# Optimization experiments

Measured on AMD Instinct MI355X. Metric: run time of the kernel, lower is better.

Reference implementation:

```python
import jax, jax.numpy as jnp
import numpy as np

NUM_HEADS = 12
GAT_HEADS = 4
EPS = 1e-5

def _ln(x, g, b):
    m = x.mean(-1, keepdims=True)
    v = ((x - m) ** 2).mean(-1, keepdims=True)
    return (x - m) / jnp.sqrt(v + EPS) * g + b

def _grid_edges(H, W, B):
    # 8-ish connectivity exactly as the Python loops build it: horizontal,
    # vertical, down-right diag, down-left diag (c>0), both directions,
    # replicated per image with node offset. Pure numpy on static shapes.
    idx = np.arange(H * W).reshape(H, W)
    p = [np.stack([idx[:, :-1].ravel(), idx[:, 1:].ravel()], 1),
         np.stack([idx[:-1, :].ravel(), idx[1:, :].ravel()], 1),
         np.stack([idx[:-1, :-1].ravel(), idx[1:, 1:].ravel()], 1),
         np.stack([idx[:-1, 1:-1].ravel(), idx[1:, :-2].ravel()], 1)]
    e = np.concatenate(p, 0)
    e = np.concatenate([e, e[:, ::-1]], 0)  # bidirectional
    e = (e[None] + (np.arange(B) * H * W)[:, None, None]).reshape(-1, 2)
    return jnp.asarray(e[:, 0]), jnp.asarray(e[:, 1])

def _forward(x, ln1_g, ln1_b, proj_w, proj_b, wqkv, bqkv, wo, bo, ln2_g, ln2_b,
             gp_w, gp_b, gat_w, att_src, att_dst, gat_b, ln3_g, ln3_b,
             mlp_w1, mlp_b1, mlp_w2, mlp_b2, fn_g, fn_b):
    B, C, H, W = x.shape
    S = H * W
    E = proj_w.shape[1]
    tok = x.reshape(B, C, S).transpose(0, 2, 1)            # [B,S,C]
    v_in = _ln(tok, ln1_g, ln1_b) @ proj_w + proj_b        # [B,S,E]
    # --- multi-head self-attention (batch_first, eval: no dropout) ---
    qkv = v_in @ wqkv + bqkv
    q, k, v = jnp.split(qkv, 3, axis=-1)
    dh = E // NUM_HEADS
    def heads(t):
        return t.reshape(B, S, NUM_HEADS, dh).transpose(0, 2, 1, 3)
    q, k, v = heads(q), heads(k), heads(v)
    att = jax.nn.softmax(jnp.einsum('bhqd,bhkd->bhqk', q, k) / jnp.sqrt(jnp.float32(dh)), axis=-1)
    o = jnp.einsum('bhqk,bhkd->bhqd', att, v).transpose(0, 2, 1, 3).reshape(B, S, E)
    x_attn = v_in + (o @ wo + bo)                          # residual
    # --- GAT over the pixel-grid graph ---
    N = B * S
    flat = x_attn.reshape(N, E)
    g = _ln(flat, ln2_g, ln2_b) @ gp_w + gp_b
    dg = E // GAT_HEADS
    hN = (g @ gat_w).reshape(N, GAT_HEADS, dg)             # [N,GH,dg]
    src, dst = _grid_edges(H, W, B)
    loops = jnp.arange(N)                                  # PyG add_self_loops=True
    src = jnp.concatenate([src, loops])
    dst = jnp.concatenate([dst, loops])
    a_s = (hN * att_src).sum(-1)                           # [N,GH]
    a_d = (hN * att_dst).sum(-1)
    e = jax.nn.leaky_relu(a_s[src] + a_d[dst], 0.2)        # [Eedges,GH]
    mseg = jax.ops.segment_max(e, dst, num_segments=N)
    ex = jnp.exp(e - mseg[dst])
    den = jax.ops.segment_sum(ex, dst, num_segments=N)
    alpha = ex / den[dst]                                  # softmax over incoming edges
    agg = jax.ops.segment_sum(hN[src] * alpha[..., None], dst, num_segments=N)
    x_gat = jax.nn.elu(agg.reshape(N, E) + gat_b)
    x_after = flat + x_gat                                 # residual
    # --- MLP block ---
    n3 = _ln(x_after, ln3_g, ln3_b)
    mlp = jax.nn.gelu(n3 @ mlp_w1 + mlp_b1, approximate=False) @ mlp_w2 + mlp_b2
    y = _ln(n3 + mlp, fn_g, fn_b)
    return y.reshape(B, H, W, E).transpose(0, 3, 1, 2)     # [B,E,H,W]

def setup_inputs() -> dict:
    key = jax.random.key(0)
    ks = jax.random.split(key, 16)
    B, C, H, W, E = 4, 2048, 32, 32, 768
    f32 = jnp.float32
    def n(k, shape, s=0.02):
        return jax.random.normal(k, shape, f32) * s
    return {
        'x': jax.random.normal(ks[0], (B, C, H, W), f32),
        'ln1_g': jnp.ones(C, f32), 'ln1_b': jnp.zeros(C, f32),
        'proj_w': n(ks[1], (C, E)), 'proj_b': jnp.zeros(E, f32),
        'wqkv': n(ks[2], (E, 3 * E)), 'bqkv': jnp.zeros(3 * E, f32),
        'wo': n(ks[3], (E, E)), 'bo': jnp.zeros(E, f32),
        'ln2_g': jnp.ones(E, f32), 'ln2_b': jnp.zeros(E, f32),
        'gp_w': n(ks[4], (E, E)), 'gp_b': jnp.zeros(E, f32),
        'gat_w': n(ks[5], (E, E)),
        'att_src': n(ks[6], (GAT_HEADS, E // GAT_HEADS), 0.1),
        'att_dst': n(ks[7], (GAT_HEADS, E // GAT_HEADS), 0.1),
        'gat_b': jnp.zeros(E, f32),
        'ln3_g': jnp.ones(E, f32), 'ln3_b': jnp.zeros(E, f32),
        'mlp_w1': n(ks[8], (E, E)), 'mlp_b1': jnp.zeros(E, f32),
        'mlp_w2': n(ks[9], (E, E)), 'mlp_b2': jnp.zeros(E, f32),
        'fn_g': jnp.ones(E, f32), 'fn_b': jnp.zeros(E, f32),
    }

def reference(x, ln1_g, ln1_b, proj_w, proj_b, wqkv, bqkv, wo, bo, ln2_g, ln2_b,
              gp_w, gp_b, gat_w, att_src, att_dst, gat_b, ln3_g, ln3_b,
              mlp_w1, mlp_b1, mlp_w2, mlp_b2, fn_g, fn_b):
    return _forward(x, ln1_g, ln1_b, proj_w, proj_b, wqkv, bqkv, wo, bo, ln2_g, ln2_b,
                    gp_w, gp_b, gat_w, att_src, att_dst, gat_b, ln3_g, ln3_b,
                    mlp_w1, mlp_b1, mlp_w2, mlp_b2, fn_g, fn_b)
```

## Files before the change

kernel.cpp:

```cpp
#include <hip/hip_runtime.h>

constexpr int Bc = 4;
constexpr int Cc = 2048;
constexpr int Sc = 1024;
constexpr int Ntok = 4096;
constexpr int Ec = 768;
constexpr int E3 = 2304;
constexpr int NHEAD = 12;
constexpr int GHEAD = 4;
constexpr int DGAT = 192;

typedef __attribute__((ext_vector_type(8))) short short8_t;
typedef __attribute__((ext_vector_type(4))) short short4_t;
typedef __attribute__((ext_vector_type(8))) unsigned short u16x8;
typedef __attribute__((ext_vector_type(4))) float f32x4;

__device__ inline unsigned short f2bf(float f) {
  unsigned int u = __builtin_bit_cast(unsigned int, f);
  u += 0x7FFFu + ((u >> 16) & 1u);
  return (unsigned short)(u >> 16);
}
__device__ inline float bf2f(unsigned short h) {
  unsigned int u = ((unsigned int)h) << 16;
  return __builtin_bit_cast(float, u);
}
__device__ inline unsigned cvtpk(float lo, float hi) {
  unsigned r;
  asm("v_cvt_pk_bf16_f32 %0, %1, %2" : "=v"(r) : "v"(lo), "v"(hi));
  return r;
}

struct WtArgs {
  const float* src[7];
  unsigned short* dst[7];
  int K[7], N[7], mode[7];
  int off[8];
};
__global__ __launch_bounds__(256) void k_wt(WtArgs a) {
  __shared__ float t[32][33];
  int bid = blockIdx.x;
  int w = 0;
  while (w < 6 && bid >= a.off[w + 1]) ++w;
  int local = bid - a.off[w];
  int K = a.K[w], N = a.N[w];
  int ntn = N >> 5;
  int tk = local / ntn, tn = local - tk * ntn;
  int k0 = tk * 32, n0 = tn * 32;
  int tx = threadIdx.x & 31, ty = threadIdx.x >> 5;
  const float* src = a.src[w];
  unsigned short* dst = a.dst[w];
  if (a.mode[w]) {
#pragma unroll
    for (int i = 0; i < 4; i++)
      dst[(size_t)(k0 + ty + i * 8) * N + n0 + tx] =
          f2bf(src[(size_t)(k0 + ty + i * 8) * N + n0 + tx]);
    return;
  }
#pragma unroll
  for (int i = 0; i < 4; i++)
    t[ty + i * 8][tx] = src[(size_t)(k0 + ty + i * 8) * N + n0 + tx];
  __syncthreads();
#pragma unroll
  for (int i = 0; i < 4; i++)
    dst[(size_t)(n0 + ty + i * 8) * K + k0 + tx] = f2bf(t[tx][ty + i * 8]);
}

__global__ __launch_bounds__(256) void k_bias2p(const float* __restrict__ gat_w,
    const float* __restrict__ gp_b, float* __restrict__ part) {
  int m = blockIdx.x * 256 + threadIdx.x;
  int jc = blockIdx.y;
  float acc = 0.f;
#pragma unroll 8
  for (int j = jc * 96; j < jc * 96 + 96; j++)
    acc += gp_b[j] * gat_w[(size_t)j * Ec + m];
  part[jc * Ec + m] = acc;
}
__global__ __launch_bounds__(256) void k_bias2r(const float* __restrict__ part,
    float* __restrict__ bias2) {
  int m = blockIdx.x * 256 + threadIdx.x;
  float acc = 0.f;
#pragma unroll
  for (int j = 0; j < 8; j++) acc += part[j * Ec + m];
  bias2[m] = acc;
}

__global__ __launch_bounds__(256) void k_ln1_stats(const float* __restrict__ x,
    float* __restrict__ psum, float* __restrict__ pss) {
  int cc = blockIdx.x, st = blockIdx.y, b = blockIdx.z;
  int sl = threadIdx.x & 15, cl = threadIdx.x >> 4;
  int s = st * 16 + sl;
  const float* xb = x + (size_t)b * Cc * Sc + s;
  float sum = 0.f, ss = 0.f;
#pragma unroll
  for (int t = 0; t < 16; t++) {
    int c = cc * 256 + cl + t * 16;
    float v = xb[(size_t)c * Sc];
    sum += v; ss += v * v;
  }
  __shared__ float rs0[16][17], rs1[16][17];
  rs0[cl][sl] = sum; rs1[cl][sl] = ss;
  __syncthreads();
  if (cl == 0) {
    float a = 0.f, q = 0.f;
#pragma unroll
    for (int i = 0; i < 16; i++) { a += rs0[i][sl]; q += rs1[i][sl]; }
    size_t bs = (size_t)(b * Sc + st * 16 + sl);
    psum[bs * 8 + cc] = a;
    pss[bs * 8 + cc] = q;
  }
}

__global__ __launch_bounds__(256) void k_ln1_norm(const float* __restrict__ x,
    const float* __restrict__ g, const float* __restrict__ bt,
    const float* __restrict__ psum, const float* __restrict__ pss,
    unsigned short* __restrict__ out) {
  int cc = blockIdx.x, st = blockIdx.y, b = blockIdx.z;
  int sl = threadIdx.x & 15, cl = threadIdx.x >> 4;
  int s = st * 16 + sl;
  __shared__ float red[16][17];
  __shared__ float mean_s[16], rstd_s[16];
  int t8 = cl;
  size_t bsrow = (size_t)(b * Sc + st * 16 + sl);
  float v = (t8 < 8) ? psum[bsrow * 8 + t8] : pss[bsrow * 8 + (t8 - 8)];
  red[t8][sl] = v;
  __syncthreads();
  if (threadIdx.x < 16) {
    float s0 = 0.f, s1 = 0.f;
#pragma unroll
    for (int i = 0; i < 8; i++) { s0 += red[i][threadIdx.x]; s1 += red[i + 8][threadIdx.x]; }
    float mean = s0 / Cc;
    mean_s[threadIdx.x] = mean;
    rstd_s[threadIdx.x] = rsqrtf(s1 / Cc - mean * mean + 1e-5f);
  }
  __syncthreads();
  float mean = mean_s[sl], rstd = rstd_s[sl];
  const float* xb = x + (size_t)b * Cc * Sc + s;
  __shared__ unsigned short Tc[16][136];
  int cb = cc * 128;
#pragma unroll
  for (int t = 0; t < 8; t++) {
    int c = cb + cl + t * 16;
    float xv = xb[(size_t)c * Sc];
    Tc[sl][cl + t * 16] = f2bf((xv - mean) * rstd * g[c] + bt[c]);
  }
  __syncthreads();
  int rl = threadIdx.x >> 4, el = threadIdx.x & 15;
  unsigned short* ob = out + ((size_t)(b * Sc) + st * 16 + rl) * Cc + cb;
  *(u16x8*)&ob[el * 8] = *(const u16x8*)&Tc[rl][el * 8];
}

template<int EPI, int OUTM>
__global__ __launch_bounds__(512) void gemm_bf16(
    const unsigned short* __restrict__ A, const unsigned short* __restrict__ Bt,
    const float* __restrict__ bias, const float* __restrict__ res,
    float* __restrict__ Cf, unsigned short* __restrict__ Cb,
    int M, int N, int K) {
  __shared__ unsigned short As[128][72];
  __shared__ unsigned short Bs[128][72];
  int tid = threadIdx.x;
  int w = tid >> 6, lane = tid & 63, g = lane >> 4, l16 = lane & 15;
  int wm = w >> 2, wn = w & 3;
  int m0 = blockIdx.y * 128, n0 = blockIdx.x * 128;
  int r0 = tid >> 3, ch0 = (tid & 7) * 8;
  int r1 = r0 + 64;
  const unsigned short* Arow0 = A + (size_t)(m0 + r0) * K + ch0;
  const unsigned short* Arow1 = A + (size_t)(m0 + r1) * K + ch0;
  const unsigned short* Brow0 = Bt + (size_t)(n0 + r0) * K + ch0;
  const unsigned short* Brow1 = Bt + (size_t)(n0 + r1) * K + ch0;
  u16x8 ra0 = *(const u16x8*)Arow0;
  u16x8 ra1 = *(const u16x8*)Arow1;
  u16x8 rb0 = *(const u16x8*)Brow0;
  u16x8 rb1 = *(const u16x8*)Brow1;
  f32x4 acc[4][2] = {};
  for (int k0 = 0; k0 < K; k0 += 64) {
    __syncthreads();
    *(u16x8*)&As[r0][ch0] = ra0;
    *(u16x8*)&As[r1][ch0] = ra1;
    *(u16x8*)&Bs[r0][ch0] = rb0;
    *(u16x8*)&Bs[r1][ch0] = rb1;
    __syncthreads();
    if (k0 + 64 < K) {
      ra0 = *(const u16x8*)(Arow0 + k0 + 64);
      ra1 = *(const u16x8*)(Arow1 + k0 + 64);
      rb0 = *(const u16x8*)(Brow0 + k0 + 64);
      rb1 = *(const u16x8*)(Brow1 + k0 + 64);
    }
#pragma unroll
    for (int ks = 0; ks < 2; ks++) {
      short8_t af[4], bf[2];
#pragma unroll
      for (int i = 0; i < 4; i++)
        af[i] = *(const short8_t*)&As[wm * 64 + i * 16 + l16][ks * 32 + g * 8];
#pragma unroll
      for (int j = 0; j < 2; j++)
        bf[j] = *(const short8_t*)&Bs[wn * 32 + j * 16 + l16][ks * 32 + g * 8];
#pragma unroll
      for (int mi = 0; mi < 4; mi++)
#pragma unroll
        for (int ni = 0; ni < 2; ni++)
          acc[mi][ni] = __builtin_amdgcn_mfma_f32_16x16x32_bf16(af[mi], bf[ni], acc[mi][ni], 0, 0, 0);
    }
  }
#pragma unroll
  for (int mi = 0; mi < 4; mi++) {
#pragma unroll
    for (int ni = 0; ni < 2; ni++) {
      int n = n0 + wn * 32 + ni * 16 + l16;
      float bv = 0.f;
      if (EPI != 0) bv = bias[n];
#pragma unroll
      for (int r = 0; r < 4; r++) {
        int m = m0 + wm * 64 + mi * 16 + g * 4 + r;
        float c = acc[mi][ni][r] + bv;
        if (EPI == 2) c += res[(size_t)m * N + n];
        if (EPI == 3) c = 0.5f * c * (1.f + erff(c * 0.70710678118f));
        if (OUTM & 1) Cf[(size_t)m * N + n] = c;
        if (OUTM & 2) Cb[(size_t)m * N + n] = f2bf(c);
      }
    }
  }
}

__global__ __launch_bounds__(256) void k_attn_mfma(const unsigned short* __restrict__ qkv,
    unsigned short* __restrict__ o) {
  __shared__ unsigned short Ks[64][72];
  __shared__ unsigned short Vs[4608];
  __shared__ unsigned short Plb[4][16][72];
  int fid = blockIdx.x;
  int xcd = fid & 7, t = fid >> 3;
  int qt = t & 15;
  int hb = (t >> 4) * 8 + xcd;
  int h = hb % NHEAD, b = hb / NHEAD;
  int tid = threadIdx.x;
  int w = tid >> 6, lane = tid & 63;
  int g = lane >> 4, l16 = lane & 15;
  const unsigned short* base  = qkv + (size_t)b * Sc * E3;
  const unsigned short* kbase = base + Ec + h * 64;
  const unsigned short* vbase = base + 2 * Ec + h * 64;
  int q0 = qt * 64 + w * 16;

  short8_t qf[2];
#pragma unroll
  for (int ks = 0; ks < 2; ks++) {
    short8_t f = *(const short8_t*)&base[(size_t)(q0 + l16) * E3 + h * 64 + ks * 32 + g * 8];
#pragma unroll
    for (int e = 0; e < 8; e++)
      f[e] = (short)f2bf(bf2f((unsigned short)f[e]) * 0.125f);
    qf[ks] = f;
  }

  int r0s = tid >> 3, ch0s = (tid & 7) * 8;
  int r1s = r0s + 32;
  int voff0 = (r0s >> 2) * 288 + (ch0s >> 4) * 72 + (r0s & 3) * 16 + ((ch0s >> 3) & 1) * 8;
  int voff1 = (r1s >> 2) * 288 + (ch0s >> 4) * 72 + (r1s & 3) * 16 + ((ch0s >> 3) & 1) * 8;
  const unsigned short* krow0 = kbase + (size_t)r0s * E3 + ch0s;
  const unsigned short* krow1 = kbase + (size_t)r1s * E3 + ch0s;
  const unsigned short* vrow0 = vbase + (size_t)r0s * E3 + ch0s;
  const unsigned short* vrow1 = vbase + (size_t)r1s * E3 + ch0s;
  constexpr size_t KTS = (size_t)64 * E3;

  u16x8 rk0 = *(const u16x8*)krow0;
  u16x8 rk1 = *(const u16x8*)krow1;
  u16x8 rv0 = *(const u16x8*)vrow0;
  u16x8 rv1 = *(const u16x8*)vrow1;

  f32x4 o_acc[4] = {};
  float m_r = -1e30f, l_r = 0.f;

  for (int kt = 0; kt < 16; kt++) {
    __syncthreads();
    *(u16x8*)&Ks[r0s][ch0s] = rk0;
    *(u16x8*)&Ks[r1s][ch0s] = rk1;
    *(u16x8*)&Vs[voff0] = rv0;
    *(u16x8*)&Vs[voff1] = rv1;
    __syncthreads();
    if (kt < 15) {
      size_t off = (size_t)(kt + 1) * KTS;
      rk0 = *(const u16x8*)(krow0 + off);
      rk1 = *(const u16x8*)(krow1 + off);
      rv0 = *(const u16x8*)(vrow0 + off);
      rv1 = *(const u16x8*)(vrow1 + off);
    }

    f32x4 s_acc[4] = {};
#pragma unroll
    for (int nt = 0; nt < 4; nt++) {
#pragma unroll
      for (int ks = 0; ks < 2; ks++) {
        short8_t kf = *(const short8_t*)&Ks[nt * 16 + l16][ks * 32 + g * 8];
        s_acc[nt] = __builtin_amdgcn_mfma_f32_16x16x32_bf16(kf, qf[ks], s_acc[nt], 0, 0, 0);
      }
    }

    float mx = s_acc[0][0];
#pragma unroll
    for (int nt = 0; nt < 4; nt++)
#pragma unroll
      for (int r = 0; r < 4; r++) mx = fmaxf(mx, s_acc[nt][r]);
    mx = fmaxf(mx, __shfl_xor(mx, 16));
    mx = fmaxf(mx, __shfl_xor(mx, 32));

    if (!__all(mx - m_r <= 8.f)) {
      float mn = fmaxf(m_r, mx);
      float sc = __expf(m_r - mn);
      m_r = mn;
      l_r *= sc;
      float osc[4];
#pragma unroll
      for (int r = 0; r < 4; r++) osc[r] = __shfl(sc, g * 4 + r);
#pragma unroll
      for (int dt = 0; dt < 4; dt++)
#pragma unroll
        for (int r = 0; r < 4; r++) o_acc[dt][r] *= osc[r];
    }

    float ts = 0.f;
#pragma unroll
    for (int nt = 0; nt < 4; nt++)
#pragma unroll
      for (int r = 0; r < 4; r++) {
        float pv = __expf(s_acc[nt][r] - m_r);
        s_acc[nt][r] = pv;
        ts += pv;
      }
    ts += __shfl_xor(ts, 16);
    ts += __shfl_xor(ts, 32);
    l_r += ts;

#pragma unroll
    for (int nt = 0; nt < 4; nt++) {
      *(unsigned*)&Plb[w][l16][nt * 16 + g * 4] = cvtpk(s_acc[nt][0], s_acc[nt][1]);
      *(unsigned*)&Plb[w][l16][nt * 16 + g * 4 + 2] = cvtpk(s_acc[nt][2], s_acc[nt][3]);
    }

#pragma unroll
    for (int ks = 0; ks < 2; ks++) {
      short8_t pf = *(const short8_t*)&Plb[w][l16][ks * 32 + g * 8];
      short4_t lo0, lo1, lo2, lo3, hi0, hi1, hi2, hi3;
      unsigned a0 = (unsigned)(uintptr_t)&Vs[(ks * 8 + g * 2) * 288 + 0 * 72 + l16] * 1u;
      unsigned a1 = a0 + 144, a2 = a0 + 288, a3 = a0 + 432;
      asm volatile("ds_read_b64_tr_b16 %0, %1" : "=v"(lo0) : "v"(a0));
      asm volatile("ds_read_b64_tr_b16 %0, %1 offset:576" : "=v"(hi0) : "v"(a0));
      asm volatile("ds_read_b64_tr_b16 %0, %1" : "=v"(lo1) : "v"(a1));
      asm volatile("ds_read_b64_tr_b16 %0, %1 offset:576" : "=v"(hi1) : "v"(a1));
      asm volatile("ds_read_b64_tr_b16 %0, %1" : "=v"(lo2) : "v"(a2));
      asm volatile("ds_read_b64_tr_b16 %0, %1 offset:576" : "=v"(hi2) : "v"(a2));
      asm volatile("ds_read_b64_tr_b16 %0, %1" : "=v"(lo3) : "v"(a3));
      asm volatile("ds_read_b64_tr_b16 %0, %1 offset:576" : "=v"(hi3) : "v"(a3));
      asm volatile("s_waitcnt lgkmcnt(0)");
      __builtin_amdgcn_sched_barrier(0);
      short4_t lo[4] = {lo0, lo1, lo2, lo3};
      short4_t hi[4] = {hi0, hi1, hi2, hi3};
#pragma unroll
      for (int dt = 0; dt < 4; dt++) {
        short8_t vf;
#pragma unroll
        for (int e = 0; e < 4; e++) { vf[e] = lo[dt][e]; vf[4 + e] = hi[dt][e]; }
        o_acc[dt] = __builtin_amdgcn_mfma_f32_16x16x32_bf16(pf, vf, o_acc[dt], 0, 0, 0);
      }
    }
  }

  float linv = 1.f / l_r;
  float inv4[4];
#pragma unroll
  for (int r = 0; r < 4; r++) inv4[r] = __shfl(linv, g * 4 + r);
  unsigned short* obase = o + (size_t)(b * Sc + q0) * Ec + h * 64;
#pragma unroll
  for (int r = 0; r < 4; r++) {
    int qrow = g * 4 + r;
#pragma unroll
    for (int dt = 0; dt < 4; dt++)
      obase[(size_t)qrow * Ec + dt * 16 + l16] = f2bf(o_acc[dt][r] * inv4[r]);
  }
}

template<int MODE>
__global__ __launch_bounds__(256) void k_lnrow(const float* __restrict__ in,
    const float* __restrict__ g, const float* __restrict__ bt,
    float* __restrict__ outf, unsigned short* __restrict__ outb) {
  int row = blockIdx.x;
  int tid = threadIdx.x;
  __shared__ float buf[Ec];
  __shared__ float rsum[4], rss[4];
  float sum = 0.f, ss = 0.f;
  for (int i = tid; i < Ec; i += 256) {
    float v = in[(size_t)row * Ec + i];
    buf[i] = v; sum += v; ss += v * v;
  }
#pragma unroll
  for (int off = 32; off > 0; off >>= 1) {
    sum += __shfl_xor(sum, off); ss += __shfl_xor(ss, off);
  }
  if ((tid & 63) == 0) { rsum[tid >> 6] = sum; rss[tid >> 6] = ss; }
  __syncthreads();
  sum = rsum[0] + rsum[1] + rsum[2] + rsum[3];
  ss = rss[0] + rss[1] + rss[2] + rss[3];
  float mean = sum / Ec;
  float rstd = rsqrtf(ss / Ec - mean * mean + 1e-5f);
  for (int i = tid; i < Ec; i += 256) {
    float v = (buf[i] - mean) * rstd * g[i] + bt[i];
    if (MODE == 2) outf[(size_t)row * Ec + i] = v;
    outb[(size_t)row * Ec + i] = f2bf(v);
  }
}

__global__ __launch_bounds__(256) void k_lnout(const float* __restrict__ in,
    const float* __restrict__ res, const float* __restrict__ g,
    const float* __restrict__ bt, float* __restrict__ out) {
  int r0 = blockIdx.x * 16;
  int b = r0 >> 10, s0 = r0 & 1023;
  __shared__ float Tr[16][772];
  __shared__ float mean_s[16], rstd_s[16];
  int rl = threadIdx.x >> 4, el = threadIdx.x & 15;
  const float* ip = in + (size_t)(r0 + rl) * Ec;
  const float* rp = res + (size_t)(r0 + rl) * Ec;
  float sum = 0.f, ss = 0.f;
  for (int i = el; i < Ec; i += 16) {
    float v = ip[i] + rp[i];
    Tr[rl][i] = v; sum += v; ss += v * v;
  }
#pragma unroll
  for (int off = 8; off; off >>= 1) {
    sum += __shfl_xor(sum, off); ss += __shfl_xor(ss, off);
  }
  if (el == 0) {
    float mean = sum / Ec;
    mean_s[rl] = mean;
    rstd_s[rl] = rsqrtf(ss / Ec - mean * mean + 1e-5f);
  }
  __syncthreads();
  int sl = threadIdx.x & 15, il = threadIdx.x >> 4;
  float mean = mean_s[sl], rstd = rstd_s[sl];
  for (int i = il; i < Ec; i += 16)
    out[((size_t)b * Ec + i) * Sc + s0 + sl] = (Tr[sl][i] - mean) * rstd * g[i] + bt[i];
}

__global__ __launch_bounds__(256) void k_asd(const unsigned short* __restrict__ hNb,
    const float* __restrict__ att_src, const float* __restrict__ att_dst,
    float* __restrict__ a_s, float* __restrict__ a_d) {
  int n = blockIdx.x * 4 + (threadIdx.x >> 6);
  int lane = threadIdx.x & 63;
  const unsigned short* hrow = hNb + (size_t)n * Ec;
#pragma unroll
  for (int h = 0; h < GHEAD; h++) {
    float ps = 0.f, pd = 0.f;
    for (int d = lane; d < DGAT; d += 64) {
      float v = bf2f(hrow[h * DGAT + d]);
      ps += v * att_src[h * DGAT + d];
      pd += v * att_dst[h * DGAT + d];
    }
#pragma unroll
    for (int off = 32; off > 0; off >>= 1) {
      ps += __shfl_xor(ps, off); pd += __shfl_xor(pd, off);
    }
    if (lane == 0) { a_s[n * GHEAD + h] = ps; a_d[n * GHEAD + h] = pd; }
  }
}

__global__ __launch_bounds__(256) void k_gat(const unsigned short* __restrict__ hNb,
    const float* __restrict__ a_s, const float* __restrict__ a_d,
    const float* __restrict__ x_attn, const float* __restrict__ gat_b,
    float* __restrict__ x_after) {
  int n = blockIdx.x;
  int b = n >> 10, s = n & 1023, r = s >> 5, c = s & 31;
  __shared__ int nbr[9];
  __shared__ float alpha[GHEAD][9];
  int tid = threadIdx.x;
  if (tid < 9) {
    int dr = tid / 3 - 1, dc = tid % 3 - 1;
    int rr = r + dr, cc = c + dc;
    int ok = (rr >= 0 && rr < 32 && cc >= 0 && cc < 32);
    if (dr == -1 && dc == 1 && cc == 31) ok = 0;
    if (dr == 1 && dc == -1 && c == 31) ok = 0;
    nbr[tid] = ok ? ((b << 10) + (rr << 5) + cc) : -1;
  }
  __syncthreads();
  if (tid < GHEAD) {
    int h = tid;
    float ad = a_d[n * GHEAD + h];
    float ev[9]; float m = -1e30f;
#pragma unroll
    for (int j = 0; j < 9; j++) {
      if (nbr[j] >= 0) {
        float e = a_s[nbr[j] * GHEAD + h] + ad;
        e = e > 0.f ? e : 0.2f * e;
        ev[j] = e; m = fmaxf(m, e);
      } else ev[j] = -1e30f;
    }
    float den = 0.f;
#pragma unroll
    for (int j = 0; j < 9; j++) {
      float x = (nbr[j] >= 0) ? expf(ev[j] - m) : 0.f;
      ev[j] = x; den += x;
    }
    float inv = 1.f / den;
#pragma unroll
    for (int j = 0; j < 9; j++) alpha[h][j] = ev[j] * inv;
  }
  __syncthreads();
  for (int e = tid; e < Ec; e += 256) {
    int h = e / DGAT;
    float acc = 0.f;
#pragma unroll
    for (int j = 0; j < 9; j++) {
      int nj = nbr[j];
      if (nj >= 0) acc += alpha[h][j] * bf2f(hNb[(size_t)nj * Ec + e]);
    }
    float v = acc + gat_b[e];
    v = v > 0.f ? v : expf(v) - 1.f;
    x_after[(size_t)n * Ec + e] = x_attn[(size_t)n * Ec + e] + v;
  }
}

extern "C" void kernel_launch(void* const* d_in, const int* in_sizes, int n_in,
                              void* d_out, int out_size, void* d_ws, size_t ws_size,
                              hipStream_t stream) {
  (void)in_sizes; (void)n_in; (void)out_size; (void)ws_size;
  const float* x      = (const float*)d_in[0];
  const float* ln1_g  = (const float*)d_in[1];
  const float* ln1_b  = (const float*)d_in[2];
  const float* proj_w = (const float*)d_in[3];
  const float* proj_b = (const float*)d_in[4];
  const float* wqkv   = (const float*)d_in[5];
  const float* bqkv   = (const float*)d_in[6];
  const float* wo     = (const float*)d_in[7];
  const float* bo     = (const float*)d_in[8];
  const float* ln2_g  = (const float*)d_in[9];
  const float* ln2_b  = (const float*)d_in[10];
  const float* gp_w   = (const float*)d_in[11];
  const float* gp_b   = (const float*)d_in[12];
  const float* gat_w  = (const float*)d_in[13];
  const float* att_src= (const float*)d_in[14];
  const float* att_dst= (const float*)d_in[15];
  const float* gat_b  = (const float*)d_in[16];
  const float* ln3_g  = (const float*)d_in[17];
  const float* ln3_b  = (const float*)d_in[18];
  const float* mlp_w1 = (const float*)d_in[19];
  const float* mlp_b1 = (const float*)d_in[20];
  const float* mlp_w2 = (const float*)d_in[21];
  const float* mlp_b2 = (const float*)d_in[22];
  const float* fn_g   = (const float*)d_in[23];
  const float* fn_b   = (const float*)d_in[24];
  float* out = (float*)d_out;

  char* p = (char*)d_ws;
  auto alloc = [&](size_t bytes) { char* q = p; p += (bytes + 255) & ~(size_t)255; return q; };
  char* regA      = alloc((size_t)Ntok * E3 * 2);
  unsigned short* n1_bf  = (unsigned short*)regA;
  unsigned short* qkv_bf = (unsigned short*)regA;
  unsigned short* proj_wt = (unsigned short*)alloc((size_t)Ec * Cc * 2);
  unsigned short* wqkv_t  = (unsigned short*)alloc((size_t)E3 * Ec * 2);
  unsigned short* wo_t    = (unsigned short*)alloc((size_t)Ec * Ec * 2);
  unsigned short* gp_bf   = (unsigned short*)alloc((size_t)Ec * Ec * 2);
  unsigned short* gat_t   = (unsigned short*)alloc((size_t)Ec * Ec * 2);
  unsigned short* m1_t    = (unsigned short*)alloc((size_t)Ec * Ec * 2);
  unsigned short* m2_t    = (unsigned short*)alloc((size_t)Ec * Ec * 2);
  unsigned short* gpgat_t = (unsigned short*)alloc((size_t)Ec * Ec * 2);
  float* bias2p = (float*)alloc((size_t)8 * Ec * 4);
  float* bias2  = (float*)alloc((size_t)Ec * 4);
  float* v_in   = (float*)alloc((size_t)Ntok * Ec * 4);
  unsigned short* v_in_bf = (unsigned short*)alloc((size_t)Ntok * Ec * 2);
  unsigned short* regE    = (unsigned short*)alloc((size_t)Ntok * Ec * 2);
  float* regF   = (float*)alloc((size_t)Ntok * Ec * 4);
  unsigned short* regG    = (unsigned short*)alloc((size_t)Ntok * Ec * 2);
  unsigned short* hN_bf   = (unsigned short*)alloc((size_t)Ntok * Ec * 2);
  float* regJ   = (float*)alloc((size_t)Ntok * Ec * 4);
  float* a_s    = (float*)alloc((size_t)Ntok * GHEAD * 4);
  float* a_d    = (float*)alloc((size_t)Ntok * GHEAD * 4);
  float* psum   = (float*)alloc((size_t)Ntok * 8 * 4);
  float* pss    = (float*)alloc((size_t)Ntok * 8 * 4);

  unsigned short* o_bf   = regE;
  unsigned short* h1_bf  = regE;
  float* x_attn = regF;
  float* n3_f   = regF;
  unsigned short* n2_bf  = regG;
  unsigned short* n3_bf  = regG;
  float* x_after = regJ;
  float* mlp_out = regJ;

  WtArgs wa;
  wa.src[0] = proj_w; wa.dst[0] = proj_wt; wa.K[0] = Cc; wa.N[0] = Ec;  wa.mode[0] = 0;
  wa.src[1] = wqkv;   wa.dst[1] = wqkv_t;  wa.K[1] = Ec; wa.N[1] = E3;  wa.mode[1] = 0;
  wa.src[2] = wo;     wa.dst[2] = wo_t;    wa.K[2] = Ec; wa.N[2] = Ec;  wa.mode[2] = 0;
  wa.src[3] = gat_w;  wa.dst[3] = gat_t;   wa.K[3] = Ec; wa.N[3] = Ec;  wa.mode[3] = 0;
  wa.src[4] = mlp_w1; wa.dst[4] = m1_t;    wa.K[4] = Ec; wa.N[4] = Ec;  wa.mode[4] = 0;
  wa.src[5] = mlp_w2; wa.dst[5] = m2_t;    wa.K[5] = Ec; wa.N[5] = Ec;  wa.mode[5] = 0;
  wa.src[6] = gp_w;   wa.dst[6] = gp_bf;   wa.K[6] = Ec; wa.N[6] = Ec;  wa.mode[6] = 1;
  int cum = 0;
  for (int i = 0; i < 7; i++) { wa.off[i] = cum; cum += (wa.K[i] >> 5) * (wa.N[i] >> 5); }
  wa.off[7] = cum;
  k_wt<<<cum, 256, 0, stream>>>(wa);

  k_bias2p<<<dim3(3, 8), 256, 0, stream>>>(gat_w, gp_b, bias2p);
  k_bias2r<<<3, 256, 0, stream>>>(bias2p, bias2);
  gemm_bf16<0, 2><<<dim3(Ec / 128, Ec / 128), 512, 0, stream>>>(
      gat_t, gp_bf, nullptr, nullptr, nullptr, gpgat_t, Ec, Ec, Ec);

  k_ln1_stats<<<dim3(8, 64, 4), 256, 0, stream>>>(x, psum, pss);
  k_ln1_norm<<<dim3(16, 64, 4), 256, 0, stream>>>(x, ln1_g, ln1_b, psum, pss, n1_bf);
  gemm_bf16<1, 3><<<dim3(Ec / 128, Ntok / 128), 512, 0, stream>>>(
      n1_bf, proj_wt, proj_b, nullptr, v_in, v_in_bf, Ntok, Ec, Cc);
  gemm_bf16<1, 2><<<dim3(E3 / 128, Ntok / 128), 512, 0, stream>>>(
      v_in_bf, wqkv_t, bqkv, nullptr, nullptr, qkv_bf, Ntok, E3, Ec);
  k_attn_mfma<<<16 * NHEAD * Bc, 256, 0, stream>>>(qkv_bf, o_bf);
  gemm_bf16<2, 1><<<dim3(Ec / 128, Ntok / 128), 512, 0, stream>>>(
      o_bf, wo_t, bo, v_in, x_attn, nullptr, Ntok, Ec, Ec);
  k_lnrow<0><<<Ntok, 256, 0, stream>>>(x_attn, ln2_g, ln2_b, nullptr, n2_bf);
  gemm_bf16<1, 2><<<dim3(Ec / 128, Ntok / 128), 512, 0, stream>>>(
      n2_bf, gpgat_t, bias2, nullptr, nullptr, hN_bf, Ntok, Ec, Ec);
  k_asd<<<Ntok / 4, 256, 0, stream>>>(hN_bf, att_src, att_dst, a_s, a_d);
  k_gat<<<Ntok, 256, 0, stream>>>(hN_bf, a_s, a_d, x_attn, gat_b, x_after);
  k_lnrow<2><<<Ntok, 256, 0, stream>>>(x_after, ln3_g, ln3_b, n3_f, n3_bf);
  gemm_bf16<3, 2><<<dim3(Ec / 128, Ntok / 128), 512, 0, stream>>>(
      n3_bf, m1_t, mlp_b1, nullptr, nullptr, h1_bf, Ntok, Ec, Ec);
  gemm_bf16<1, 1><<<dim3(Ec / 128, Ntok / 128), 512, 0, stream>>>(
      h1_bf, m2_t, mlp_b2, nullptr, mlp_out, nullptr, Ntok, Ec, Ec);
  k_lnout<<<256, 256, 0, stream>>>(n3_f, mlp_out, fn_g, fn_b, out);
}
```

Baseline: 256.2 us.

## Add 64x128-tile GEMM for N=768 layers and fuse GAT score kernels

```diff
diff --git a/kernel.cpp b/kernel.cpp
--- a/kernel.cpp
+++ b/kernel.cpp
@@ -221,6 +221,85 @@
   }
 }
 
+template<int EPI, int OUTM>
+__global__ __launch_bounds__(256) void gemm64_bf16(
+    const unsigned short* __restrict__ A, const unsigned short* __restrict__ Bt,
+    const float* __restrict__ bias, const float* __restrict__ res,
+    float* __restrict__ Cf, unsigned short* __restrict__ Cb,
+    int M, int N, int K) {
+  __shared__ unsigned short As[64][72];
+  __shared__ unsigned short Bs[128][72];
+  int tid = threadIdx.x;
+  int w = tid >> 6, lane = tid & 63, g = lane >> 4, l16 = lane & 15;
+  int wm = w >> 1, wn = w & 1;
+  int m0 = blockIdx.y * 64, n0 = blockIdx.x * 128;
+  int r0 = tid >> 3, ch0 = (tid & 7) * 8;
+  const unsigned short* ArowA = A + (size_t)(m0 + r0) * K + ch0;
+  const unsigned short* ArowB = A + (size_t)(m0 + r0 + 32) * K + ch0;
+  const unsigned short* Brow0 = Bt + (size_t)(n0 + r0) * K + ch0;
+  const unsigned short* Brow1 = Bt + (size_t)(n0 + r0 + 32) * K + ch0;
+  const unsigned short* Brow2 = Bt + (size_t)(n0 + r0 + 64) * K + ch0;
+  const unsigned short* Brow3 = Bt + (size_t)(n0 + r0 + 96) * K + ch0;
+  u16x8 raA = *(const u16x8*)ArowA;
+  u16x8 raB = *(const u16x8*)ArowB;
+  u16x8 rb0 = *(const u16x8*)Brow0;
+  u16x8 rb1 = *(const u16x8*)Brow1;
+  u16x8 rb2 = *(const u16x8*)Brow2;
+  u16x8 rb3 = *(const u16x8*)Brow3;
+  f32x4 acc[2][4] = {};
+  for (int k0 = 0; k0 < K; k0 += 64) {
+    __syncthreads();
+    *(u16x8*)&As[r0][ch0] = raA;
+    *(u16x8*)&As[r0 + 32][ch0] = raB;
+    *(u16x8*)&Bs[r0][ch0] = rb0;
+    *(u16x8*)&Bs[r0 + 32][ch0] = rb1;
+    *(u16x8*)&Bs[r0 + 64][ch0] = rb2;
+    *(u16x8*)&Bs[r0 + 96][ch0] = rb3;
+    __syncthreads();
+    if (k0 + 64 < K) {
+      raA = *(const u16x8*)(ArowA + k0 + 64);
+      raB = *(const u16x8*)(ArowB + k0 + 64);
+      rb0 = *(const u16x8*)(Brow0 + k0 + 64);
+      rb1 = *(const u16x8*)(Brow1 + k0 + 64);
+      rb2 = *(const u16x8*)(Brow2 + k0 + 64);
+      rb3 = *(const u16x8*)(Brow3 + k0 + 64);
+    }
+#pragma unroll
+    for (int ks = 0; ks < 2; ks++) {
+      short8_t af[2], bf[4];
+#pragma unroll
+      for (int i = 0; i < 2; i++)
+        af[i] = *(const short8_t*)&As[wm * 32 + i * 16 + l16][ks * 32 + g * 8];
+#pragma unroll
+      for (int j = 0; j < 4; j++)
+        bf[j] = *(const short8_t*)&Bs[wn * 64 + j * 16 + l16][ks * 32 + g * 8];
+#pragma unroll
+      for (int mi = 0; mi < 2; mi++)
+#pragma unroll
+        for (int ni = 0; ni < 4; ni++)
+          acc[mi][ni] = __builtin_amdgcn_mfma_f32_16x16x32_bf16(af[mi], bf[ni], acc[mi][ni], 0, 0, 0);
+    }
+  }
+#pragma unroll
+  for (int mi = 0; mi < 2; mi++) {
+#pragma unroll
+    for (int ni = 0; ni < 4; ni++) {
+      int n = n0 + wn * 64 + ni * 16 + l16;
+      float bv = 0.f;
+      if (EPI != 0) bv = bias[n];
+#pragma unroll
+      for (int r = 0; r < 4; r++) {
+        int m = m0 + wm * 32 + mi * 16 + g * 4 + r;
+        float c = acc[mi][ni][r] + bv;
+        if (EPI == 2) c += res[(size_t)m * N + n];
+        if (EPI == 3) c = 0.5f * c * (1.f + erff(c * 0.70710678118f));
+        if (OUTM & 1) Cf[(size_t)m * N + n] = c;
+        if (OUTM & 2) Cb[(size_t)m * N + n] = f2bf(c);
+      }
+    }
+  }
+}
+
 __global__ __launch_bounds__(256) void k_attn_mfma(const unsigned short* __restrict__ qkv,
     unsigned short* __restrict__ o) {
   __shared__ unsigned short Ks[64][72];
@@ -436,35 +515,14 @@
     out[((size_t)b * Ec + i) * Sc + s0 + sl] = (Tr[sl][i] - mean) * rstd * g[i] + bt[i];
 }
 
-__global__ __launch_bounds__(256) void k_asd(const unsigned short* __restrict__ hNb,
+__global__ __launch_bounds__(256) void k_gatfull(const unsigned short* __restrict__ hNb,
     const float* __restrict__ att_src, const float* __restrict__ att_dst,
-    float* __restrict__ a_s, float* __restrict__ a_d) {
-  int n = blockIdx.x * 4 + (threadIdx.x >> 6);
-  int lane = threadIdx.x & 63;
-  const unsigned short* hrow = hNb + (size_t)n * Ec;
-#pragma unroll
-  for (int h = 0; h < GHEAD; h++) {
-    float ps = 0.f, pd = 0.f;
-    for (int d = lane; d < DGAT; d += 64) {
-      float v = bf2f(hrow[h * DGAT + d]);
-      ps += v * att_src[h * DGAT + d];
-      pd += v * att_dst[h * DGAT + d];
-    }
-#pragma unroll
-    for (int off = 32; off > 0; off >>= 1) {
-      ps += __shfl_xor(ps, off); pd += __shfl_xor(pd, off);
-    }
-    if (lane == 0) { a_s[n * GHEAD + h] = ps; a_d[n * GHEAD + h] = pd; }
-  }
-}
-
-__global__ __launch_bounds__(256) void k_gat(const unsigned short* __restrict__ hNb,
-    const float* __restrict__ a_s, const float* __restrict__ a_d,
     const float* __restrict__ x_attn, const float* __restrict__ gat_b,
     float* __restrict__ x_after) {
   int n = blockIdx.x;
   int b = n >> 10, s = n & 1023, r = s >> 5, c = s & 31;
   __shared__ int nbr[9];
+  __shared__ unsigned short hrows[9][Ec];
   __shared__ float alpha[GHEAD][9];
   int tid = threadIdx.x;
   if (tid < 9) {
@@ -476,27 +534,57 @@
     nbr[tid] = ok ? ((b << 10) + (rr << 5) + cc) : -1;
   }
   __syncthreads();
-  if (tid < GHEAD) {
-    int h = tid;
-    float ad = a_d[n * GHEAD + h];
-    float ev[9]; float m = -1e30f;
+  for (int i = tid; i < 9 * 96; i += 256) {
+    int j = i / 96, e8 = i - j * 96;
+    if (nbr[j] >= 0)
+      *(u16x8*)&hrows[j][e8 * 8] = *(const u16x8*)&hNb[(size_t)nbr[j] * Ec + e8 * 8];
+  }
+  __syncthreads();
+  int w = tid >> 6, lane = tid & 63;
+  {
+    float pd = 0.f;
+#pragma unroll
+    for (int t = 0; t < 3; t++) {
+      int d = w * DGAT + lane + t * 64;
+      pd += bf2f(hrows[4][d]) * att_dst[d];
+    }
+#pragma unroll
+    for (int off = 32; off; off >>= 1) pd += __shfl_xor(pd, off);
+    float as_j[9];
 #pragma unroll
     for (int j = 0; j < 9; j++) {
+      float p = 0.f;
       if (nbr[j] >= 0) {
-        float e = a_s[nbr[j] * GHEAD + h] + ad;
-        e = e > 0.f ? e : 0.2f * e;
-        ev[j] = e; m = fmaxf(m, e);
-      } else ev[j] = -1e30f;
-    }
-    float den = 0.f;
-#pragma unroll
-    for (int j = 0; j < 9; j++) {
-      float x = (nbr[j] >= 0) ? expf(ev[j] - m) : 0.f;
-      ev[j] = x; den += x;
-    }
-    float inv = 1.f / den;
-#pragma unroll
-    for (int j = 0; j < 9; j++) alpha[h][j] = ev[j] * inv;
+#pragma unroll
+        for (int t = 0; t < 3; t++) {
+          int d = w * DGAT + lane + t * 64;
+          p += bf2f(hrows[j][d]) * att_src[d];
+        }
+      }
+#pragma unroll
+      for (int off = 32; off; off >>= 1) p += __shfl_xor(p, off);
+      as_j[j] = p;
+    }
+    if (lane == 0) {
+      float ev[9]; float m = -1e30f;
+#pragma unroll
+      for (int j = 0; j < 9; j++) {
+        if (nbr[j] >= 0) {
+          float e = as_j[j] + pd;
+          e = e > 0.f ? e : 0.2f * e;
+          ev[j] = e; m = fmaxf(m, e);
+        } else ev[j] = -1e30f;
+      }
+      float den = 0.f;
+#pragma unroll
+      for (int j = 0; j < 9; j++) {
+        float xv = (nbr[j] >= 0) ? expf(ev[j] - m) : 0.f;
+        ev[j] = xv; den += xv;
+      }
+      float inv = 1.f / den;
+#pragma unroll
+      for (int j = 0; j < 9; j++) alpha[w][j] = ev[j] * inv;
+    }
   }
   __syncthreads();
   for (int e = tid; e < Ec; e += 256) {
@@ -504,8 +592,7 @@
     float acc = 0.f;
 #pragma unroll
     for (int j = 0; j < 9; j++) {
-      int nj = nbr[j];
-      if (nj >= 0) acc += alpha[h][j] * bf2f(hNb[(size_t)nj * Ec + e]);
+      if (nbr[j] >= 0) acc += alpha[h][j] * bf2f(hrows[j][e]);
     }
     float v = acc + gat_b[e];
     v = v > 0.f ? v : expf(v) - 1.f;
@@ -566,8 +653,6 @@
   unsigned short* regG    = (unsigned short*)alloc((size_t)Ntok * Ec * 2);
   unsigned short* hN_bf   = (unsigned short*)alloc((size_t)Ntok * Ec * 2);
   float* regJ   = (float*)alloc((size_t)Ntok * Ec * 4);
-  float* a_s    = (float*)alloc((size_t)Ntok * GHEAD * 4);
-  float* a_d    = (float*)alloc((size_t)Ntok * GHEAD * 4);
   float* psum   = (float*)alloc((size_t)Ntok * 8 * 4);
   float* pss    = (float*)alloc((size_t)Ntok * 8 * 4);
 
@@ -595,27 +680,26 @@
 
   k_bias2p<<<dim3(3, 8), 256, 0, stream>>>(gat_w, gp_b, bias2p);
   k_bias2r<<<3, 256, 0, stream>>>(bias2p, bias2);
-  gemm_bf16<0, 2><<<dim3(Ec / 128, Ec / 128), 512, 0, stream>>>(
+  gemm64_bf16<0, 2><<<dim3(Ec / 128, Ec / 64), 256, 0, stream>>>(
       gat_t, gp_bf, nullptr, nullptr, nullptr, gpgat_t, Ec, Ec, Ec);
 
   k_ln1_stats<<<dim3(8, 64, 4), 256, 0, stream>>>(x, psum, pss);
   k_ln1_norm<<<dim3(16, 64, 4), 256, 0, stream>>>(x, ln1_g, ln1_b, psum, pss, n1_bf);
-  gemm_bf16<1, 3><<<dim3(Ec / 128, Ntok / 128), 512, 0, stream>>>(
+  gemm64_bf16<1, 3><<<dim3(Ec / 128, Ntok / 64), 256, 0, stream>>>(
       n1_bf, proj_wt, proj_b, nullptr, v_in, v_in_bf, Ntok, Ec, Cc);
   gemm_bf16<1, 2><<<dim3(E3 / 128, Ntok / 128), 512, 0, stream>>>(
       v_in_bf, wqkv_t, bqkv, nullptr, nullptr, qkv_bf, Ntok, E3, Ec);
   k_attn_mfma<<<16 * NHEAD * Bc, 256, 0, stream>>>(qkv_bf, o_bf);
-  gemm_bf16<2, 1><<<dim3(Ec / 128, Ntok / 128), 512, 0, stream>>>(
+  gemm64_bf16<2, 1><<<dim3(Ec / 128, Ntok / 64), 256, 0, stream>>>(
       o_bf, wo_t, bo, v_in, x_attn, nullptr, Ntok, Ec, Ec);
   k_lnrow<0><<<Ntok, 256, 0, stream>>>(x_attn, ln2_g, ln2_b, nullptr, n2_bf);
-  gemm_bf16<1, 2><<<dim3(Ec / 128, Ntok / 128), 512, 0, stream>>>(
+  gemm64_bf16<1, 2><<<dim3(Ec / 128, Ntok / 64), 256, 0, stream>>>(
       n2_bf, gpgat_t, bias2, nullptr, nullptr, hN_bf, Ntok, Ec, Ec);
-  k_asd<<<Ntok / 4, 256, 0, stream>>>(hN_bf, att_src, att_dst, a_s, a_d);
-  k_gat<<<Ntok, 256, 0, stream>>>(hN_bf, a_s, a_d, x_attn, gat_b, x_after);
+  k_gatfull<<<Ntok, 256, 0, stream>>>(hN_bf, att_src, att_dst, x_attn, gat_b, x_after);
   k_lnrow<2><<<Ntok, 256, 0, stream>>>(x_after, ln3_g, ln3_b, n3_f, n3_bf);
-  gemm_bf16<3, 2><<<dim3(Ec / 128, Ntok / 128), 512, 0, stream>>>(
+  gemm64_bf16<3, 2><<<dim3(Ec / 128, Ntok / 64), 256, 0, stream>>>(
       n3_bf, m1_t, mlp_b1, nullptr, nullptr, h1_bf, Ntok, Ec, Ec);
-  gemm_bf16<1, 1><<<dim3(Ec / 128, Ntok / 128), 512, 0, stream>>>(
+  gemm64_bf16<1, 1><<<dim3(Ec / 128, Ntok / 64), 256, 0, stream>>>(
       h1_bf, m2_t, mlp_b2, nullptr, mlp_out, nullptr, Ntok, Ec, Ec);
   k_lnout<<<256, 256, 0, stream>>>(n3_f, mlp_out, fn_g, fn_b, out);
 }
```

Result: no change. 253.9 us (-0.9%).
